# Kernel optimization log

Measured on AMD Instinct MI355X. Metric: run time of the kernel, lower is better.

The kernel has to match this reference:

```python
import jax, jax.numpy as jnp
import numpy as np

NEG_SLOPE = 0.2


def setup_inputs() -> dict:
    key = jax.random.key(0)
    ks = jax.random.split(key, 9)
    N, E, D, H, C, G = 50000, 800000, 128, 4, 32, 64
    x = jax.random.normal(ks[0], (N, D), dtype=jnp.float32)
    edge_index = jax.random.randint(ks[1], (2, E), 0, N, dtype=jnp.int64)
    batch_ids = jnp.sort(jax.random.randint(ks[2], (N,), 0, G, dtype=jnp.int64))
    Wl = jax.random.normal(ks[3], (D, H * C), dtype=jnp.float32) / np.sqrt(D)
    Wr = jax.random.normal(ks[4], (D, H * C), dtype=jnp.float32) / np.sqrt(D)
    att = jax.random.normal(ks[5], (H, C), dtype=jnp.float32) / np.sqrt(C)
    bias_conv = jax.random.normal(ks[6], (H * C,), dtype=jnp.float32) * 0.01
    W_mlp = jax.random.normal(ks[7], (H * C, H * C), dtype=jnp.float32) / np.sqrt(H * C)
    b_mlp = jax.random.normal(ks[8], (H * C,), dtype=jnp.float32) * 0.01
    return {"x": x, "edge_index": edge_index, "batch_ids": batch_ids,
            "num_graphs": G, "Wl": Wl, "Wr": Wr, "att": att,
            "bias_conv": bias_conv, "W_mlp": W_mlp, "b_mlp": b_mlp}


def gatv2_forward(x, edge_index, batch_ids, num_graphs, Wl, Wr, att, bias_conv, W_mlp, b_mlp):
    N = x.shape[0]
    H, C = att.shape
    # add self loops (PyG default)
    loops = jnp.arange(N, dtype=edge_index.dtype)
    src = jnp.concatenate([edge_index[0], loops])
    dst = jnp.concatenate([edge_index[1], loops])
    xl = (x @ Wl).reshape(N, H, C)  # source transform
    xr = (x @ Wr).reshape(N, H, C)  # target transform
    # GATv2 attention logits per edge/head
    e = jax.nn.leaky_relu(xl[src] + xr[dst], NEG_SLOPE)  # [E,H,C]
    logits = jnp.einsum('ehc,hc->eh', e, att)            # [E,H]
    # segment softmax over incoming edges of each dst node
    m = jax.ops.segment_max(logits, dst, num_segments=N)
    ex = jnp.exp(logits - m[dst])
    denom = jax.ops.segment_sum(ex, dst, num_segments=N)
    alpha = ex / denom[dst]                              # [E,H]
    # weighted scatter-sum of source features
    out = jax.ops.segment_sum(alpha[:, :, None] * xl[src], dst, num_segments=N)
    out = out.reshape(N, H * C) + bias_conv
    out = jax.nn.relu(out)
    # global max pool per graph
    pooled = jax.ops.segment_max(out, batch_ids, num_segments=num_graphs)
    return jax.nn.relu(pooled @ W_mlp + b_mlp)


def reference(x, edge_index, batch_ids, num_graphs, Wl, Wr, att, bias_conv, W_mlp, b_mlp):
    return gatv2_forward(x, edge_index, batch_ids, num_graphs, Wl, Wr, att,
                         bias_conv, W_mlp, b_mlp)
```

## Files before the change

kernel.cpp:

```cpp
#include <hip/hip_runtime.h>
#include <hip/hip_bf16.h>

#define NN 50000
#define EE 800000
#define HC 128
#define GG 64

#define NBLK 256
#define CHUNK (EE / NBLK)
#define NBUCK ((NN + 63) >> 6)
#define NTOT (NBUCK * NBLK)
#define NSB ((NTOT + 1023) / 1024)
#define ECAP 2048

typedef __attribute__((ext_vector_type(8))) short bf16x8;
typedef __attribute__((ext_vector_type(4))) float f32x4;
typedef _Float16 hv2 __attribute__((ext_vector_type(2)));

__device__ __forceinline__ float dpp4_redrow(float t) {
  t += __int_as_float(__builtin_amdgcn_update_dpp(0, __float_as_int(t), 0x111, 0xf, 0xf, true));
  t += __int_as_float(__builtin_amdgcn_update_dpp(0, __float_as_int(t), 0x112, 0xf, 0xf, true));
  t += __int_as_float(__builtin_amdgcn_update_dpp(0, __float_as_int(t), 0x114, 0xf, 0xf, true));
  t += __int_as_float(__builtin_amdgcn_update_dpp(0, __float_as_int(t), 0x118, 0xf, 0xf, true));
  return t;
}
__device__ __forceinline__ float bcast15(float t) {
  return __int_as_float(__builtin_amdgcn_ds_swizzle(__float_as_int(t), 0x1F0));
}

__device__ __forceinline__ unsigned pkbf(float lo, float hi) {
  __hip_bfloat162 h = __float22bfloat162_rn(float2{lo, hi});
  return *reinterpret_cast<unsigned*>(&h);
}

__device__ __forceinline__ void proc2h(unsigned wa, unsigned wb, hv2 att2, hv2 xr2,
                                       float& s, float& a0, float& a1) {
  hv2 va = __builtin_bit_cast(hv2, wa);
  hv2 vb = __builtin_bit_cast(hv2, wb);
  hv2 ya = va + xr2, yb = vb + xr2;
  hv2 la = __builtin_elementwise_max(ya, ya * (_Float16)0.2f);
  hv2 lb = __builtin_elementwise_max(yb, yb * (_Float16)0.2f);
  float ta = __builtin_amdgcn_fdot2(la, att2, 0.f, false);
  float tb = __builtin_amdgcn_fdot2(lb, att2, 0.f, false);
  ta = dpp4_redrow(ta); tb = dpp4_redrow(tb);
  float pa = __builtin_amdgcn_exp2f(bcast15(ta));
  float pb = __builtin_amdgcn_exp2f(bcast15(tb));
  s += pa + pb;
  a0 = fmaf(pa, (float)va.x, a0); a1 = fmaf(pa, (float)va.y, a1);
  a0 = fmaf(pb, (float)vb.x, a0); a1 = fmaf(pb, (float)vb.y, a1);
}

__global__ __launch_bounds__(128) void prep_w(const float* __restrict__ Wl,
                                              const float* __restrict__ Wr,
                                              short* __restrict__ Wtb) {
  int c = blockIdx.x;
  int k = threadIdx.x;
  const float* W = (c < 128) ? Wl : Wr;
  float v = W[k * 128 + (c & 127)];
  Wtb[c * 128 + k] = (short)(pkbf(v, 0.f) & 0xFFFF);
}

__global__ __launch_bounds__(256) void gemm_xw(
    const float* __restrict__ x, const short* __restrict__ Wtb,
    _Float16* __restrict__ xlh, _Float16* __restrict__ xrh)
{
  __shared__ short xs[128 * 136];
  const int t = threadIdx.x;
  const int rowbase = blockIdx.x * 128;
  const int y = blockIdx.y;
#pragma unroll
  for (int i = 0; i < 16; ++i) {
    int fi = i * 256 + t;
    int row = fi >> 5, k4 = fi & 31;
    int ar = rowbase + row; if (ar >= NN) ar = NN - 1;
    float4 v = *(const float4*)(x + (size_t)ar * 128 + k4 * 4);
    uint2 p = { pkbf(v.x, v.y), pkbf(v.z, v.w) };
    *(uint2*)&xs[row * 136 + k4 * 4] = p;
  }
  __syncthreads();
  const int w = t >> 6, l = t & 63;
  const int lo16 = l & 15, hi = l >> 4;
  f32x4 acc[2][8];
#pragma unroll
  for (int rf = 0; rf < 2; ++rf)
#pragma unroll
    for (int cf = 0; cf < 8; ++cf) acc[rf][cf] = f32x4{0.f, 0.f, 0.f, 0.f};

  const short* __restrict__ wp = Wtb + (size_t)y * 128 * 128;
  const short* asrc0 = &xs[(w * 32 + lo16) * 136 + hi * 8];
  const short* asrc1 = asrc0 + 16 * 136;
#pragma unroll
  for (int ks = 0; ks < 4; ++ks) {
    bf16x8 a0 = *(const bf16x8*)(asrc0 + ks * 32);
    bf16x8 a1 = *(const bf16x8*)(asrc1 + ks * 32);
#pragma unroll
    for (int cf = 0; cf < 8; ++cf) {
      bf16x8 b = *(const bf16x8*)&wp[(cf * 16 + lo16) * 128 + ks * 32 + hi * 8];
      acc[0][cf] = __builtin_amdgcn_mfma_f32_16x16x32_bf16(a0, b, acc[0][cf], 0, 0, 0);
      acc[1][cf] = __builtin_amdgcn_mfma_f32_16x16x32_bf16(a1, b, acc[1][cf], 0, 0, 0);
    }
  }
  _Float16* __restrict__ dst = y == 0 ? xlh : xrh;
#pragma unroll
  for (int rf = 0; rf < 2; ++rf)
#pragma unroll
    for (int cf = 0; cf < 8; ++cf)
#pragma unroll
      for (int r = 0; r < 4; ++r) {
        int row = rowbase + w * 32 + rf * 16 + hi * 4 + r;
        if (row < NN) {
          int col = cf * 16 + lo16;
          dst[(size_t)row * 128 + col] = (_Float16)acc[rf][cf][r];
        }
      }
}

__global__ __launch_bounds__(256) void hist_coarse(const int* __restrict__ ei,
                                                   int* __restrict__ H2) {
  __shared__ int h[NBUCK];
  int t = threadIdx.x, blk = blockIdx.x;
  for (int b = t; b < NBUCK; b += 256) h[b] = 0;
  __syncthreads();
  int e0 = blk * CHUNK;
  for (int i = t; i < CHUNK; i += 256) {
    int d = ei[EE + e0 + i];
    atomicAdd(&h[d >> 6], 1);
  }
  __syncthreads();
  for (int b = t; b < NBUCK; b += 256) H2[blk * NBUCK + b] = h[b];
}

__global__ __launch_bounds__(256) void scanA(const int* __restrict__ H2,
                                             int* __restrict__ PS, int* __restrict__ bsum) {
  __shared__ int tmp[256];
  int t = threadIdx.x;
  int base = blockIdx.x * 1024 + t * 4;
  int v[4], local = 0;
#pragma unroll
  for (int j = 0; j < 4; ++j) {
    int L = base + j;
    v[j] = (L < NTOT) ? H2[(L % NBLK) * NBUCK + (L / NBLK)] : 0;
    local += v[j];
  }
  tmp[t] = local; __syncthreads();
  for (int off = 1; off < 256; off <<= 1) {
    int xv = (t >= off) ? tmp[t - off] : 0; __syncthreads();
    tmp[t] += xv; __syncthreads();
  }
  int excl = tmp[t] - local;
#pragma unroll
  for (int j = 0; j < 4; ++j) { int L = base + j; if (L < NTOT) PS[L] = excl; excl += v[j]; }
  if (t == 255) bsum[blockIdx.x] = tmp[255];
}

__global__ void scanB(int* __restrict__ bsum) {
  __shared__ int tmp[256];
  int t = threadIdx.x;
  int v = (t < NSB) ? bsum[t] : 0;
  tmp[t] = v; __syncthreads();
  for (int off = 1; off < 256; off <<= 1) {
    int xv = (t >= off) ? tmp[t - off] : 0; __syncthreads();
    tmp[t] += xv; __syncthreads();
  }
  if (t < NSB) bsum[t] = tmp[t] - v;
}

__global__ __launch_bounds__(256) void scatter_coarse(const int* __restrict__ ei,
                                                      const int* __restrict__ PS,
                                                      const int* __restrict__ bsum,
                                                      int* __restrict__ ec) {
  __shared__ int colbase[NBUCK];
  __shared__ int cur[NBUCK];
  int t = threadIdx.x, blk = blockIdx.x;
  for (int b = t; b < NBUCK; b += 256) {
    int L = b * NBLK + blk;
    colbase[b] = PS[L] + bsum[L >> 10];
    cur[b] = 0;
  }
  __syncthreads();
  int e0 = blk * CHUNK;
  for (int i = t; i < CHUNK; i += 256) {
    int d = ei[EE + e0 + i], s = ei[e0 + i];
    int b = d >> 6;
    int r = atomicAdd(&cur[b], 1);
    ec[colbase[b] + r] = s | ((d & 63) << 16);
  }
}

__global__ __launch_bounds__(256) void fine_sort(const int* __restrict__ PS,
                                                 const int* __restrict__ bsum,
                                                 const int* __restrict__ ec,
                                                 int* __restrict__ rs, int* __restrict__ csr) {
  __shared__ int lbuf[ECAP];
  __shared__ int outb[ECAP + 64];
  __shared__ int fh[64], sexcl[65], cur2[64];
  int t = threadIdx.x, b = blockIdx.x;
  int L0 = b * NBLK;
  int start = PS[L0] + bsum[L0 >> 10];
  int end;
  if (b + 1 < NBUCK) { int L1 = (b + 1) * NBLK; end = PS[L1] + bsum[L1 >> 10]; }
  else end = EE;
  int node0 = b << 6;
  int nl = NN - node0; if (nl > 64) nl = 64;
  int cnt = end - start; if (cnt > ECAP) cnt = ECAP;
  if (t < 64) { fh[t] = 0; cur2[t] = 0; }
  __syncthreads();
  for (int i = t; i < cnt; i += 256) {
    int p = ec[start + i];
    lbuf[i] = p;
    atomicAdd(&fh[(p >> 16) & 63], 1);
  }
  __syncthreads();
  if (t < 64) {
    int val = fh[t] + (t < nl ? 1 : 0);
    int w = val;
    for (int off = 1; off < 64; off <<= 1) {
      int u = __shfl_up(w, off);
      if (t >= off) w += u;
    }
    sexcl[t] = w - val;
    if (t == 63) sexcl[64] = w;
  }
  __syncthreads();
  int base = start + node0;
  if (t <= nl) rs[node0 + t] = base + sexcl[t];
  if (t < nl) {
    int r = atomicAdd(&cur2[t], 1);
    outb[sexcl[t] + r] = node0 + t;
  }
  for (int i = t; i < cnt; i += 256) {
    int p = lbuf[i];
    int f = (p >> 16) & 63;
    int r = atomicAdd(&cur2[f], 1);
    outb[sexcl[f] + r] = p & 0xFFFF;
  }
  __syncthreads();
  int tot = cnt + nl;
  for (int i = t; i < tot; i += 256) csr[base + i] = outb[i];
}

__global__ __launch_bounds__(256) void gat_agg(
    const unsigned* __restrict__ xlu, const unsigned* __restrict__ xru,
    const int* __restrict__ rs, const int* __restrict__ csr,
    const float* __restrict__ att, const float* __restrict__ bias,
    float* __restrict__ outn)
{
  int wid = threadIdx.x >> 6, lane = threadIdx.x & 63;
  int n = blockIdx.x * 4 + wid;
  if (n >= NN) return;
  hv2 xr2 = __builtin_bit_cast(hv2, xru[n * 64 + lane]);
  float2 at2 = ((const float2*)att)[lane];
  const float LOG2E = 1.4426950408889634f;
  hv2 att2;
  att2.x = (_Float16)(at2.x * LOG2E);
  att2.y = (_Float16)(at2.y * LOG2E);
  float s = 0.f, a0 = 0.f, a1 = 0.f;

  int jbeg = rs[n], jend = rs[n + 1];
  for (int j0 = jbeg; j0 < jend; j0 += 64) {
    int cnt = jend - j0; if (cnt > 64) cnt = 64;
    int sj = csr[j0 + (lane < cnt ? lane : cnt - 1)];
    int base = 0;
    for (; base + 8 <= cnt; base += 8) {
      int e0 = __builtin_amdgcn_readlane(sj, base + 0);
      int e1 = __builtin_amdgcn_readlane(sj, base + 1);
      int e2 = __builtin_amdgcn_readlane(sj, base + 2);
      int e3 = __builtin_amdgcn_readlane(sj, base + 3);
      int e4 = __builtin_amdgcn_readlane(sj, base + 4);
      int e5 = __builtin_amdgcn_readlane(sj, base + 5);
      int e6 = __builtin_amdgcn_readlane(sj, base + 6);
      int e7 = __builtin_amdgcn_readlane(sj, base + 7);
      unsigned w0 = xlu[e0 * 64 + lane];
      unsigned w1 = xlu[e1 * 64 + lane];
      unsigned w2 = xlu[e2 * 64 + lane];
      unsigned w3 = xlu[e3 * 64 + lane];
      unsigned w4 = xlu[e4 * 64 + lane];
      unsigned w5 = xlu[e5 * 64 + lane];
      unsigned w6 = xlu[e6 * 64 + lane];
      unsigned w7 = xlu[e7 * 64 + lane];
      proc2h(w0, w1, att2, xr2, s, a0, a1);
      proc2h(w2, w3, att2, xr2, s, a0, a1);
      proc2h(w4, w5, att2, xr2, s, a0, a1);
      proc2h(w6, w7, att2, xr2, s, a0, a1);
    }
    for (; base + 2 <= cnt; base += 2) {
      int e0 = __builtin_amdgcn_readlane(sj, base + 0);
      int e1 = __builtin_amdgcn_readlane(sj, base + 1);
      unsigned w0 = xlu[e0 * 64 + lane];
      unsigned w1 = xlu[e1 * 64 + lane];
      proc2h(w0, w1, att2, xr2, s, a0, a1);
    }
    if (base < cnt) {
      int e0 = __builtin_amdgcn_readlane(sj, base);
      unsigned w0 = xlu[e0 * 64 + lane];
      hv2 va = __builtin_bit_cast(hv2, w0);
      hv2 ya = va + xr2;
      hv2 la = __builtin_elementwise_max(ya, ya * (_Float16)0.2f);
      float t = __builtin_amdgcn_fdot2(la, att2, 0.f, false);
      t = dpp4_redrow(t);
      float p = __builtin_amdgcn_exp2f(bcast15(t));
      s += p;
      a0 = fmaf(p, (float)va.x, a0); a1 = fmaf(p, (float)va.y, a1);
    }
  }
  float inv = 1.f / s;
  float2 bi = ((const float2*)bias)[lane];
  float2 o;
  o.x = fmaxf(fmaf(a0, inv, bi.x), 0.f);
  o.y = fmaxf(fmaf(a1, inv, bi.y), 0.f);
  ((float2*)outn)[n * 64 + lane] = o;
}

__global__ __launch_bounds__(128) void pool_max(const float* __restrict__ outn,
                                                const int* __restrict__ batch,
                                                unsigned int* __restrict__ pooled) {
  int c = threadIdx.x;
  int n0 = blockIdx.x * 128;
  int nend = n0 + 128; if (nend > NN) nend = NN;
  int curg = batch[n0];
  float mx = 0.f;
#pragma unroll 4
  for (int n = n0; n < nend; ++n) {
    int g = batch[n];
    if (g != curg) {
      atomicMax(&pooled[curg * HC + c], __float_as_uint(mx));
      mx = 0.f; curg = g;
    }
    mx = fmaxf(mx, outn[(size_t)n * HC + c]);
  }
  atomicMax(&pooled[curg * HC + c], __float_as_uint(mx));
}

__global__ __launch_bounds__(128) void mlp_out(const unsigned int* __restrict__ pooled,
                                               const float* __restrict__ W,
                                               const float* __restrict__ b,
                                               float* __restrict__ out) {
  __shared__ float p[128];
  int g = blockIdx.x, j = threadIdx.x;
  p[j] = __uint_as_float(pooled[g * HC + j]);
  __syncthreads();
  float acc = b[j];
#pragma unroll 8
  for (int k = 0; k < 128; ++k) acc = fmaf(p[k], W[k * 128 + j], acc);
  out[g * HC + j] = fmaxf(acc, 0.f);
}

extern "C" void kernel_launch(void* const* d_in, const int* in_sizes, int n_in,
                              void* d_out, int out_size, void* d_ws, size_t ws_size,
                              hipStream_t stream) {
  const float* x    = (const float*)d_in[0];
  const int*   ei   = (const int*)d_in[1];
  const int*   batch= (const int*)d_in[2];
  const float* Wl   = (const float*)d_in[4];
  const float* Wr   = (const float*)d_in[5];
  const float* att  = (const float*)d_in[6];
  const float* bias = (const float*)d_in[7];
  const float* Wm   = (const float*)d_in[8];
  const float* bm   = (const float*)d_in[9];

  char* ws = (char*)d_ws;
  size_t off = 0;
  auto alloc = [&](size_t bytes) { void* p = ws + off; off += (bytes + 255) & ~size_t(255); return p; };
  unsigned* xlu  = (unsigned*)alloc((size_t)NN * 64 * 4);
  unsigned* xru  = (unsigned*)alloc((size_t)NN * 64 * 4);
  float* outn    = (float*)alloc((size_t)NN * HC * 4);
  int*   rs      = (int*)alloc((size_t)(NN + 1) * 4);
  int*   csr     = (int*)alloc((size_t)(EE + NN) * 4);
  int*   bsum    = (int*)alloc(NSB * 4);
  short* Wtb     = (short*)alloc((size_t)256 * 128 * 2);
  unsigned int* pooled = (unsigned int*)alloc((size_t)GG * HC * 4);
  int* ec = (int*)outn;
  int* H2 = (int*)((char*)outn + (size_t)4 * 1024 * 1024);
  int* PS = (int*)((char*)outn + (size_t)6 * 1024 * 1024);

  (void)hipMemsetAsync(pooled, 0, (size_t)GG * HC * 4, stream);

  prep_w<<<256, 128, 0, stream>>>(Wl, Wr, Wtb);
  gemm_xw<<<dim3((NN + 127) / 128, 2), 256, 0, stream>>>(x, Wtb, (_Float16*)xlu, (_Float16*)xru);
  hist_coarse<<<NBLK, 256, 0, stream>>>(ei, H2);
  scanA<<<NSB, 256, 0, stream>>>(H2, PS, bsum);
  scanB<<<1, 256, 0, stream>>>(bsum);
  scatter_coarse<<<NBLK, 256, 0, stream>>>(ei, PS, bsum, ec);
  fine_sort<<<NBUCK, 256, 0, stream>>>(PS, bsum, ec, rs, csr);
  gat_agg<<<NN / 4, 256, 0, stream>>>(xlu, xru, rs, csr, att, bias, outn);
  pool_max<<<(NN + 127) / 128, 128, 0, stream>>>(outn, batch, pooled);
  mlp_out<<<GG, 128, 0, stream>>>(pooled, Wm, bm, (float*)d_out);
}
```

Measured before the change: 145.8 us.

## Fuse Wl/Wr GEMMs per block and replace row reduction with rotate-sum DPP

The GEMM kernel now computes both the xl and xr projections in a single block, so the converted bf16 tile of x is loaded once instead of twice. This halves the x reads and the conversion work, at the cost of more accumulator registers and half as many blocks. In the aggregation kernel, the 16-lane reduction uses row_ror DPP so every lane ends with the full sum, which removes the ds_swizzle broadcast. Gather address computation is also restructured to scalar base pointers.

New measurement: 158.0 us. 1.08x slower.

```diff
diff --git a/kernel.cpp b/kernel.cpp
--- a/kernel.cpp
+++ b/kernel.cpp
@@ -17,15 +17,12 @@
 typedef __attribute__((ext_vector_type(4))) float f32x4;
 typedef _Float16 hv2 __attribute__((ext_vector_type(2)));
 
-__device__ __forceinline__ float dpp4_redrow(float t) {
-  t += __int_as_float(__builtin_amdgcn_update_dpp(0, __float_as_int(t), 0x111, 0xf, 0xf, true));
-  t += __int_as_float(__builtin_amdgcn_update_dpp(0, __float_as_int(t), 0x112, 0xf, 0xf, true));
-  t += __int_as_float(__builtin_amdgcn_update_dpp(0, __float_as_int(t), 0x114, 0xf, 0xf, true));
-  t += __int_as_float(__builtin_amdgcn_update_dpp(0, __float_as_int(t), 0x118, 0xf, 0xf, true));
+__device__ __forceinline__ float dpp4_rorsum(float t) {
+  t += __int_as_float(__builtin_amdgcn_update_dpp(__float_as_int(t), __float_as_int(t), 0x121, 0xf, 0xf, false));
+  t += __int_as_float(__builtin_amdgcn_update_dpp(__float_as_int(t), __float_as_int(t), 0x122, 0xf, 0xf, false));
+  t += __int_as_float(__builtin_amdgcn_update_dpp(__float_as_int(t), __float_as_int(t), 0x124, 0xf, 0xf, false));
+  t += __int_as_float(__builtin_amdgcn_update_dpp(__float_as_int(t), __float_as_int(t), 0x128, 0xf, 0xf, false));
   return t;
-}
-__device__ __forceinline__ float bcast15(float t) {
-  return __int_as_float(__builtin_amdgcn_ds_swizzle(__float_as_int(t), 0x1F0));
 }
 
 __device__ __forceinline__ unsigned pkbf(float lo, float hi) {
@@ -42,9 +39,8 @@
   hv2 lb = __builtin_elementwise_max(yb, yb * (_Float16)0.2f);
   float ta = __builtin_amdgcn_fdot2(la, att2, 0.f, false);
   float tb = __builtin_amdgcn_fdot2(lb, att2, 0.f, false);
-  ta = dpp4_redrow(ta); tb = dpp4_redrow(tb);
-  float pa = __builtin_amdgcn_exp2f(bcast15(ta));
-  float pb = __builtin_amdgcn_exp2f(bcast15(tb));
+  float pa = __builtin_amdgcn_exp2f(dpp4_rorsum(ta));
+  float pb = __builtin_amdgcn_exp2f(dpp4_rorsum(tb));
   s += pa + pb;
   a0 = fmaf(pa, (float)va.x, a0); a1 = fmaf(pa, (float)va.y, a1);
   a0 = fmaf(pb, (float)vb.x, a0); a1 = fmaf(pb, (float)vb.y, a1);
@@ -67,7 +63,6 @@
   __shared__ short xs[128 * 136];
   const int t = threadIdx.x;
   const int rowbase = blockIdx.x * 128;
-  const int y = blockIdx.y;
 #pragma unroll
   for (int i = 0; i < 16; ++i) {
     int fi = i * 256 + t;
@@ -80,13 +75,15 @@
   __syncthreads();
   const int w = t >> 6, l = t & 63;
   const int lo16 = l & 15, hi = l >> 4;
-  f32x4 acc[2][8];
+  f32x4 accL[2][8], accR[2][8];
 #pragma unroll
   for (int rf = 0; rf < 2; ++rf)
 #pragma unroll
-    for (int cf = 0; cf < 8; ++cf) acc[rf][cf] = f32x4{0.f, 0.f, 0.f, 0.f};
-
-  const short* __restrict__ wp = Wtb + (size_t)y * 128 * 128;
+    for (int cf = 0; cf < 8; ++cf) {
+      accL[rf][cf] = f32x4{0.f, 0.f, 0.f, 0.f};
+      accR[rf][cf] = f32x4{0.f, 0.f, 0.f, 0.f};
+    }
+
   const short* asrc0 = &xs[(w * 32 + lo16) * 136 + hi * 8];
   const short* asrc1 = asrc0 + 16 * 136;
 #pragma unroll
@@ -95,12 +92,15 @@
     bf16x8 a1 = *(const bf16x8*)(asrc1 + ks * 32);
 #pragma unroll
     for (int cf = 0; cf < 8; ++cf) {
-      bf16x8 b = *(const bf16x8*)&wp[(cf * 16 + lo16) * 128 + ks * 32 + hi * 8];
-      acc[0][cf] = __builtin_amdgcn_mfma_f32_16x16x32_bf16(a0, b, acc[0][cf], 0, 0, 0);
-      acc[1][cf] = __builtin_amdgcn_mfma_f32_16x16x32_bf16(a1, b, acc[1][cf], 0, 0, 0);
-    }
-  }
-  _Float16* __restrict__ dst = y == 0 ? xlh : xrh;
+      const short* bp = &Wtb[(cf * 16 + lo16) * 128 + ks * 32 + hi * 8];
+      bf16x8 bL = *(const bf16x8*)bp;
+      bf16x8 bR = *(const bf16x8*)(bp + 128 * 128);
+      accL[0][cf] = __builtin_amdgcn_mfma_f32_16x16x32_bf16(a0, bL, accL[0][cf], 0, 0, 0);
+      accL[1][cf] = __builtin_amdgcn_mfma_f32_16x16x32_bf16(a1, bL, accL[1][cf], 0, 0, 0);
+      accR[0][cf] = __builtin_amdgcn_mfma_f32_16x16x32_bf16(a0, bR, accR[0][cf], 0, 0, 0);
+      accR[1][cf] = __builtin_amdgcn_mfma_f32_16x16x32_bf16(a1, bR, accR[1][cf], 0, 0, 0);
+    }
+  }
 #pragma unroll
   for (int rf = 0; rf < 2; ++rf)
 #pragma unroll
@@ -110,7 +110,8 @@
         int row = rowbase + w * 32 + rf * 16 + hi * 4 + r;
         if (row < NN) {
           int col = cf * 16 + lo16;
-          dst[(size_t)row * 128 + col] = (_Float16)acc[rf][cf][r];
+          xlh[(size_t)row * 128 + col] = (_Float16)accL[rf][cf][r];
+          xrh[(size_t)row * 128 + col] = (_Float16)accR[rf][cf][r];
         }
       }
 }
@@ -262,43 +263,42 @@
     int sj = csr[j0 + (lane < cnt ? lane : cnt - 1)];
     int base = 0;
     for (; base + 8 <= cnt; base += 8) {
-      int e0 = __builtin_amdgcn_readlane(sj, base + 0);
-      int e1 = __builtin_amdgcn_readlane(sj, base + 1);
-      int e2 = __builtin_amdgcn_readlane(sj, base + 2);
-      int e3 = __builtin_amdgcn_readlane(sj, base + 3);
-      int e4 = __builtin_amdgcn_readlane(sj, base + 4);
-      int e5 = __builtin_amdgcn_readlane(sj, base + 5);
-      int e6 = __builtin_amdgcn_readlane(sj, base + 6);
-      int e7 = __builtin_amdgcn_readlane(sj, base + 7);
-      unsigned w0 = xlu[e0 * 64 + lane];
-      unsigned w1 = xlu[e1 * 64 + lane];
-      unsigned w2 = xlu[e2 * 64 + lane];
-      unsigned w3 = xlu[e3 * 64 + lane];
-      unsigned w4 = xlu[e4 * 64 + lane];
-      unsigned w5 = xlu[e5 * 64 + lane];
-      unsigned w6 = xlu[e6 * 64 + lane];
-      unsigned w7 = xlu[e7 * 64 + lane];
+      const unsigned* p0 = xlu + 64 * __builtin_amdgcn_readlane(sj, base + 0);
+      const unsigned* p1 = xlu + 64 * __builtin_amdgcn_readlane(sj, base + 1);
+      const unsigned* p2 = xlu + 64 * __builtin_amdgcn_readlane(sj, base + 2);
+      const unsigned* p3 = xlu + 64 * __builtin_amdgcn_readlane(sj, base + 3);
+      const unsigned* p4 = xlu + 64 * __builtin_amdgcn_readlane(sj, base + 4);
+      const unsigned* p5 = xlu + 64 * __builtin_amdgcn_readlane(sj, base + 5);
+      const unsigned* p6 = xlu + 64 * __builtin_amdgcn_readlane(sj, base + 6);
+      const unsigned* p7 = xlu + 64 * __builtin_amdgcn_readlane(sj, base + 7);
+      unsigned w0 = p0[lane];
+      unsigned w1 = p1[lane];
+      unsigned w2 = p2[lane];
+      unsigned w3 = p3[lane];
+      unsigned w4 = p4[lane];
+      unsigned w5 = p5[lane];
+      unsigned w6 = p6[lane];
+      unsigned w7 = p7[lane];
       proc2h(w0, w1, att2, xr2, s, a0, a1);
       proc2h(w2, w3, att2, xr2, s, a0, a1);
       proc2h(w4, w5, att2, xr2, s, a0, a1);
       proc2h(w6, w7, att2, xr2, s, a0, a1);
     }
     for (; base + 2 <= cnt; base += 2) {
-      int e0 = __builtin_amdgcn_readlane(sj, base + 0);
-      int e1 = __builtin_amdgcn_readlane(sj, base + 1);
-      unsigned w0 = xlu[e0 * 64 + lane];
-      unsigned w1 = xlu[e1 * 64 + lane];
+      const unsigned* p0 = xlu + 64 * __builtin_amdgcn_readlane(sj, base + 0);
+      const unsigned* p1 = xlu + 64 * __builtin_amdgcn_readlane(sj, base + 1);
+      unsigned w0 = p0[lane];
+      unsigned w1 = p1[lane];
       proc2h(w0, w1, att2, xr2, s, a0, a1);
     }
     if (base < cnt) {
-      int e0 = __builtin_amdgcn_readlane(sj, base);
-      unsigned w0 = xlu[e0 * 64 + lane];
+      const unsigned* p0 = xlu + 64 * __builtin_amdgcn_readlane(sj, base);
+      unsigned w0 = p0[lane];
       hv2 va = __builtin_bit_cast(hv2, w0);
       hv2 ya = va + xr2;
       hv2 la = __builtin_elementwise_max(ya, ya * (_Float16)0.2f);
       float t = __builtin_amdgcn_fdot2(la, att2, 0.f, false);
-      t = dpp4_redrow(t);
-      float p = __builtin_amdgcn_exp2f(bcast15(t));
+      float p = __builtin_amdgcn_exp2f(dpp4_rorsum(t));
       s += p;
       a0 = fmaf(p, (float)va.x, a0); a1 = fmaf(p, (float)va.y, a1);
     }
@@ -376,7 +376,7 @@
   (void)hipMemsetAsync(pooled, 0, (size_t)GG * HC * 4, stream);
 
   prep_w<<<256, 128, 0, stream>>>(Wl, Wr, Wtb);
-  gemm_xw<<<dim3((NN + 127) / 128, 2), 256, 0, stream>>>(x, Wtb, (_Float16*)xlu, (_Float16*)xru);
+  gemm_xw<<<(NN + 127) / 128, 256, 0, stream>>>(x, Wtb, (_Float16*)xlu, (_Float16*)xru);
   hist_coarse<<<NBLK, 256, 0, stream>>>(ei, H2);
   scanA<<<NSB, 256, 0, stream>>>(H2, PS, bsum);
   scanB<<<1, 256, 0, stream>>>(bsum);
```
